# Kernel tuning notes

Hardware: AMD Instinct MI355X
Metric: run time of the kernel (lower is better)

The kernel has to match this reference:

```python
import jax, jax.numpy as jnp
import numpy as np
from jax import lax

EPS = 1e-10

def _ln(x, g, b):
    m = x.mean(-1, keepdims=True)
    v = x.var(-1, keepdims=True)
    return (x - m) / jnp.sqrt(v + 1e-5) * g + b

def _gather(t, idx):
    # t: (B, HW, c), idx: (B, HW, d) -> (B, HW, d, c); out[n,i,k,:] = t[n, idx[n,i,k], :]
    return jax.vmap(lambda tn, In: tn[In])(t, idx)

def setup_inputs() -> dict:
    key = jax.random.key(0)
    ks = jax.random.split(key, 20)
    b, v, c, d, h, w, hid, ksz = 2, 2, 128, 64, 64, 64, 256, 5
    hw = h * w
    Bf = b * v  # v_1 == 1 target view per reference view
    std = 0.02
    return {
        'features_mv': jax.random.normal(ks[0], (b, v, c, h, w), jnp.float32),
        'warp_indices': jax.random.randint(ks[1], (Bf, hw, d), 0, hw, jnp.int32),
        'depth_prob': jax.random.uniform(ks[2], (Bf, hw, d), jnp.float32),
        'ln1_g': jnp.ones((c,), jnp.float32), 'ln1_b': jnp.zeros((c,), jnp.float32),
        'wq': jax.random.normal(ks[3], (c, c), jnp.float32) * std, 'bq': jnp.zeros((c,), jnp.float32),
        'wk': jax.random.normal(ks[4], (c, c), jnp.float32) * std, 'bk': jnp.zeros((c,), jnp.float32),
        'wv': jax.random.normal(ks[5], (c, c), jnp.float32) * std, 'bv': jnp.zeros((c,), jnp.float32),
        'k_pe': jax.random.normal(ks[6], (1, 1, d), jnp.float32) * std,
        'v_pe': jax.random.normal(ks[7], (1, 1, d), jnp.float32) * std,
        'rpe': jax.random.normal(ks[8], (1, 1, d), jnp.float32) * std,
        'proj_w': jax.random.normal(ks[9], (c, c), jnp.float32) * std, 'proj_b': jnp.zeros((c,), jnp.float32),
        'ln2_g': jnp.ones((c,), jnp.float32), 'ln2_b': jnp.zeros((c,), jnp.float32),
        'fc1_w': jax.random.normal(ks[10], (c, hid), jnp.float32) * std, 'fc1_b': jnp.zeros((hid,), jnp.float32),
        'dw_w': jax.random.normal(ks[11], (hid, 1, ksz, ksz), jnp.float32) * std, 'dw_b': jnp.zeros((hid,), jnp.float32),
        'fc2_w': jax.random.normal(ks[12], (hid, c), jnp.float32) * std, 'fc2_b': jnp.zeros((c,), jnp.float32),
    }

def reference(features_mv, warp_indices, depth_prob, ln1_g, ln1_b, wq, bq, wk, bk, wv, bv,
              k_pe, v_pe, rpe, proj_w, proj_b, ln2_g, ln2_b, fc1_w, fc1_b, dw_w, dw_b, fc2_w, fc2_b):
    b, v, c, h, w = features_mv.shape
    hw = h * w
    hid = fc1_w.shape[1]
    scale = c ** (-0.5)  # num_heads = 1 -> head_dim = dim

    # (b v) (h w) c
    x = features_mv.reshape(b * v, c, hw).transpose(0, 2, 1)
    shortcut = x
    xn = _ln(x, ln1_g, ln1_b)
    q = xn @ wq + bq
    k = xn @ wk + bk
    vv = xn @ wv + bv

    # nn pairing: v=2, v_1=1 -> each reference view attends the other view
    Q = (q.reshape(b, v, hw, c) * scale).reshape(b * v, hw, c)
    K = k.reshape(b, v, hw, c)[:, ::-1].reshape(b * v, hw, c)
    V = vv.reshape(b, v, hw, c)[:, ::-1].reshape(b * v, hw, c)

    # SMM_QmK: cost[n,i,k] = sum_c Q[n,i,c] * K[n, idx[n,i,k], c]
    Kg = _gather(K, warp_indices)                       # (B, hw, d, c)
    cost = jnp.einsum('bic,bikc->bik', Q, Kg)
    Q_pe = Q.sum(-1, keepdims=True)                     # (B, hw, 1)
    cost = cost + Q_pe * k_pe + rpe                     # broadcast (1,1,d)

    # (Sim_UNet similarity refinement omitted: UNetModel source unavailable; identity here)
    attn = jax.nn.softmax(cost, axis=-1)
    attn = attn * depth_prob
    attn = (attn + EPS) / (attn.sum(-1, keepdims=True) + EPS)

    # SMM_AmV: out[n,i,c] = sum_k attn[n,i,k] * V[n, idx[n,i,k], c]
    Vg = _gather(V, warp_indices)                       # (B, hw, d, c)
    out = jnp.einsum('bik,bikc->bic', attn, Vg)
    out = out + (attn * v_pe).sum(-1, keepdims=True)

    # projection + residual (v_1 == 1 so B == b*v)
    x = shortcut + (out @ proj_w + proj_b)

    # ConvFFN residual branch
    xn2 = _ln(x, ln2_g, ln2_b)
    y = jax.nn.gelu(xn2 @ fc1_w + fc1_b, approximate=False)
    yi = y.transpose(0, 2, 1).reshape(b * v, hid, h, w)
    yc = lax.conv_general_dilated(yi, dw_w, (1, 1), 'SAME', feature_group_count=hid,
                                  dimension_numbers=('NCHW', 'OIHW', 'NCHW'))
    yc = jax.nn.gelu(yc + dw_b[None, :, None, None], approximate=False)
    y = y + yc.reshape(b * v, hid, hw).transpose(0, 2, 1)
    y = y @ fc2_w + fc2_b
    return x + y
```

## Files before the change

### kernel.cpp

```cpp
#include <hip/hip_runtime.h>
#include <math.h>

#define TOK   16384
#define HW    4096
#define C     128
#define D     64
#define HID   256

constexpr float LN_EPS = 1e-5f;
constexpr float EPS_R  = 1e-10f;
constexpr float QSCALE = 0.08838834764831845f;

typedef __attribute__((ext_vector_type(8))) short  bf16x8;
typedef __attribute__((ext_vector_type(4))) float  f32x4;
typedef __attribute__((ext_vector_type(2))) _Float16 half2v;
#define MFMA16(a, b, c) __builtin_amdgcn_mfma_f32_16x16x32_bf16((a), (b), (c), 0, 0, 0)

__device__ __forceinline__ float bflo(unsigned u) { return __uint_as_float(u << 16); }
__device__ __forceinline__ float bfhi(unsigned u) { return __uint_as_float(u & 0xffff0000u); }
__device__ __forceinline__ float bfu(unsigned short u) { return __uint_as_float((unsigned)u << 16); }
__device__ __forceinline__ unsigned short f2bf(float f) {
  unsigned u = __float_as_uint(f);
  unsigned r = (u + 0x7fffu + ((u >> 16) & 1u)) >> 16;
  return (unsigned short)r;
}
__device__ __forceinline__ unsigned short f2h(float f) {
  _Float16 h = (_Float16)f;
  unsigned short r;
  __builtin_memcpy(&r, &h, 2);
  return r;
}
__device__ __forceinline__ float gelu_exact(float x) {
  return 0.5f * x * (1.0f + erff(x * 0.7071067811865476f));
}

union U4H { uint4 v; half2v h[4]; };
union U1H { unsigned v; half2v h; };

#if __has_builtin(__builtin_amdgcn_fdot2)
__device__ __forceinline__ float dot2h(half2v a, half2v b, float c) {
  return __builtin_amdgcn_fdot2(a, b, c, false);
}
#else
__device__ __forceinline__ float dot2h(half2v a, half2v b, float c) {
  return c + (float)a.x * (float)b.x + (float)a.y * (float)b.y;
}
#endif

__global__ __launch_bounds__(256) void k_prepln1(const float* __restrict__ wq,
    const float* __restrict__ wk, const float* __restrict__ wv,
    const float* __restrict__ pw, const float* __restrict__ f1w,
    const float* __restrict__ f2w, unsigned short* __restrict__ wt,
    const float* __restrict__ feat, const float* __restrict__ g,
    const float* __restrict__ b, unsigned short* __restrict__ xnb) {
  __shared__ float tile[64][C + 1];
  int bidx = blockIdx.x;
  if (bidx < 512) {
    int id = bidx * 256 + threadIdx.x;
    if (id < 16384) {
      int n = id >> 7, k = id & 127;
      wt[id] = f2bf(wq[k * 128 + n]);
    } else if (id < 32768) {
      int e = id - 16384; int n = e >> 7, k = e & 127;
      wt[id] = f2bf(wk[k * 128 + n]);
    } else if (id < 49152) {
      int e = id - 32768; int n = e >> 7, k = e & 127;
      wt[id] = f2bf(wv[k * 128 + n]);
    } else if (id < 65536) {
      int e = id - 49152; int n = e >> 7, k = e & 127;
      wt[id] = f2bf(pw[k * 128 + n]);
    } else if (id < 98304) {
      int e = id - 65536; int n = e >> 7, k = e & 127;
      wt[id] = f2bf(f1w[k * 256 + n]);
    } else {
      int e = id - 98304; int n = e >> 8, k = e & 255;
      wt[id] = f2bf(f2w[k * 128 + n]);
    }
    return;
  }
  int t0 = (bidx - 512) * 64;
  int n = t0 / HW, i0 = t0 % HW;
  int tid = threadIdx.x;
  const float* fb = feat + (size_t)n * C * HW;
  for (int e = tid; e < 64 * C; e += 256) {
    int ch = e >> 6, ii = e & 63;
    tile[ii][ch] = fb[(size_t)ch * HW + i0 + ii];
  }
  __syncthreads();
  int wave = tid >> 6, lane = tid & 63;
  for (int tkn = wave; tkn < 64; tkn += 4) {
    float a0 = tile[tkn][lane];
    float a1 = tile[tkn][lane + 64];
    float s = a0 + a1;
    for (int off = 32; off; off >>= 1) s += __shfl_xor(s, off, 64);
    float mean = s * (1.0f / 128.0f);
    float d0 = a0 - mean, d1 = a1 - mean;
    float v = d0 * d0 + d1 * d1;
    for (int off = 32; off; off >>= 1) v += __shfl_xor(v, off, 64);
    float rstd = rsqrtf(v * (1.0f / 128.0f) + LN_EPS);
    size_t ro = (size_t)(t0 + tkn) * C;
    xnb[ro + lane]      = f2bf(d0 * rstd * g[lane] + b[lane]);
    xnb[ro + lane + 64] = f2bf(d1 * rstd * g[lane + 64] + b[lane + 64]);
  }
}

__global__ __launch_bounds__(256) void k_qkv(const unsigned short* __restrict__ xnb,
    const unsigned short* __restrict__ wt,
    const float* __restrict__ bq, const float* __restrict__ bk,
    const float* __restrict__ bv, unsigned short* __restrict__ qh,
    unsigned short* __restrict__ ksw, unsigned short* __restrict__ vsw) {
  int w = threadIdx.x >> 6, lane = threadIdx.x & 63;
  int q4 = lane >> 4, m = lane & 15;
  int t0 = blockIdx.x * 64 + w * 16;
  int wsel = blockIdx.y;
  const unsigned short* Wt = wt + wsel * 16384;
  const unsigned short* ap = xnb + (size_t)(t0 + m) * C + q4 * 8;
  bf16x8 a[4];
  #pragma unroll
  for (int ks = 0; ks < 4; ks++) a[ks] = *(const bf16x8*)(ap + ks * 32);
  f32x4 acc[8];
  #pragma unroll
  for (int nt = 0; nt < 8; nt++) acc[nt] = (f32x4){0.f, 0.f, 0.f, 0.f};
  #pragma unroll
  for (int nt = 0; nt < 8; nt++) {
    const unsigned short* bp = Wt + (size_t)(nt * 16 + m) * C + q4 * 8;
    #pragma unroll
    for (int ks = 0; ks < 4; ks++) {
      bf16x8 bfrag = *(const bf16x8*)(bp + ks * 32);
      acc[nt] = MFMA16(a[ks], bfrag, acc[nt]);
    }
  }
  const float* B = (wsel == 0) ? bq : ((wsel == 1) ? bk : bv);
  float sc = (wsel == 0) ? QSCALE : 1.0f;
  unsigned short* O = (wsel == 0) ? qh : ((wsel == 1) ? ksw : vsw);
  int n = t0 >> 12, i0 = t0 & 4095;
  int base = (wsel == 0) ? t0 : (((n ^ 1) << 12) + i0);
  #pragma unroll
  for (int nt = 0; nt < 8; nt++) {
    int col = nt * 16 + m;
    float bb = B[col];
    #pragma unroll
    for (int reg = 0; reg < 4; reg++) {
      int row = base + q4 * 4 + reg;
      O[(size_t)row * C + col] = f2h((acc[nt][reg] + bb) * sc);
    }
  }
}

__global__ __launch_bounds__(256) void k_attn_proj_fc1(
    const unsigned short* __restrict__ qh, const unsigned short* __restrict__ ksw,
    const unsigned short* __restrict__ vsw, const int* __restrict__ widx,
    const float* __restrict__ dprob, const float* __restrict__ kpe,
    const float* __restrict__ vpe, const float* __restrict__ rpe,
    const unsigned short* __restrict__ wt, const float* __restrict__ pb,
    const float* __restrict__ feat, float* __restrict__ xio,
    const float* __restrict__ g2, const float* __restrict__ b2,
    const float* __restrict__ f1b, unsigned short* __restrict__ y) {
  __shared__ unsigned short axn[16 * C];
  __shared__ float ps1[4][16];
  __shared__ float ps2[4][16];
  int lane = threadIdx.x & 63;
  int wave = threadIdx.x >> 6;
  int bid = blockIdx.x;
  int n = (bid >> 1) & 3;
  int within = ((bid >> 3) << 1) | (bid & 1);
  int T0 = n * HW + within * 16;
  const unsigned short* Kb = ksw + (size_t)n * HW * C;
  const unsigned short* Vb = vsw + (size_t)n * HW * C;
  int gg = lane >> 3, s = lane & 7;
  half2v ones = {(_Float16)1.0f, (_Float16)1.0f};

  for (int tj = 0; tj < 4; ++tj) {
    int token = T0 + wave * 4 + tj;
    int myidx = widx[(size_t)token * D + lane];
    float mydp = dprob[(size_t)token * D + lane];
    half2v qreg[8];
    {
      const unsigned short* qp = qh + (size_t)token * C + s * 16;
      U4H qa, qb2;
      qa.v = *(const uint4*)(qp);
      qb2.v = *(const uint4*)(qp + 8);
      #pragma unroll
      for (int i = 0; i < 4; i++) { qreg[i] = qa.h[i]; qreg[4 + i] = qb2.h[i]; }
    }
    float qpe = 0.f;
    #pragma unroll
    for (int i = 0; i < 8; i++) qpe = dot2h(qreg[i], ones, qpe);
    qpe += __shfl_xor(qpe, 1, 64);
    qpe += __shfl_xor(qpe, 2, 64);
    qpe += __shfl_xor(qpe, 4, 64);
    int rowv[8];
    #pragma unroll
    for (int pass = 0; pass < 8; ++pass)
      rowv[pass] = __shfl(myidx, pass * 8 + gg, 64);
    uint4 ka[8], kb[8];
    #pragma unroll
    for (int pass = 0; pass < 8; ++pass) {
      const unsigned short* kr = Kb + (size_t)rowv[pass] * C + s * 16;
      ka[pass] = *(const uint4*)(kr);
      kb[pass] = *(const uint4*)(kr + 8);
    }
    float mycost = 0.f;
    #pragma unroll
    for (int pass = 0; pass < 8; ++pass) {
      U4H ua, ub;
      ua.v = ka[pass]; ub.v = kb[pass];
      float p = 0.f;
      #pragma unroll
      for (int i = 0; i < 4; i++) p = dot2h(ua.h[i], qreg[i], p);
      #pragma unroll
      for (int i = 0; i < 4; i++) p = dot2h(ub.h[i], qreg[4 + i], p);
      p += __shfl_xor(p, 1, 64);
      p += __shfl_xor(p, 2, 64);
      p += __shfl_xor(p, 4, 64);
      float t = __shfl(p, (lane & 7) << 3, 64);
      if (pass == gg) mycost = t;
    }
    mycost += qpe * kpe[lane] + rpe[lane];
    float mx = mycost;
    for (int off = 32; off; off >>= 1) mx = fmaxf(mx, __shfl_xor(mx, off, 64));
    float e = __expf(mycost - mx);
    float ssum = e;
    for (int off = 32; off; off >>= 1) ssum += __shfl_xor(ssum, off, 64);
    float attn = (e / ssum) * mydp;
    float sren = attn;
    for (int off = 32; off; off >>= 1) sren += __shfl_xor(sren, off, 64);
    attn = (attn + EPS_R) / (sren + EPS_R);
    float vpt = attn * vpe[lane];
    for (int off = 32; off; off >>= 1) vpt += __shfl_xor(vpt, off, 64);
    float o0 = vpt, o1 = vpt;
    unsigned att_u = __float_as_uint(attn);
    #pragma unroll
    for (int blk = 0; blk < 8; ++blk) {
      unsigned vv[8];
      #pragma unroll
      for (int j = 0; j < 8; j++) {
        int row = __builtin_amdgcn_readlane(myidx, blk * 8 + j);
        vv[j] = *(const unsigned*)(Vb + (size_t)row * C + lane * 2);
      }
      #pragma unroll
      for (int j = 0; j < 8; j++) {
        float a = __uint_as_float(__builtin_amdgcn_readlane(att_u, blk * 8 + j));
        U1H h; h.v = vv[j];
        o0 += a * (float)h.h.x;
        o1 += a * (float)h.h.y;
      }
    }
    unsigned pk = (unsigned)f2bf(o0) | ((unsigned)f2bf(o1) << 16);
    int row = wave * 4 + tj;
    int boff = row * 256 + lane * 4;
    boff ^= (row & 15) << 4;
    *(unsigned*)((char*)axn + boff) = pk;
  }
  __syncthreads();

  int q4 = lane >> 4, m = lane & 15;
  bf16x8 a[4];
  #pragma unroll
  for (int ks = 0; ks < 4; ks++) {
    int boff = m * 256 + ks * 64 + q4 * 16;
    boff ^= m << 4;
    a[ks] = *(const bf16x8*)((char*)axn + boff);
  }
  const unsigned short* Wp = wt + 3 * 16384;
  f32x4 acc[2];
  #pragma unroll
  for (int nt = 0; nt < 2; nt++) acc[nt] = (f32x4){0.f, 0.f, 0.f, 0.f};
  #pragma unroll
  for (int nt = 0; nt < 2; nt++) {
    int colt = wave * 32 + nt * 16;
    const unsigned short* bp = Wp + (size_t)(colt + m) * C + q4 * 8;
    #pragma unroll
    for (int ks = 0; ks < 4; ks++) {
      bf16x8 bfrag = *(const bf16x8*)(bp + ks * 32);
      acc[nt] = MFMA16(a[ks], bfrag, acc[nt]);
    }
  }
  int ibase = (T0 & 4095) + q4 * 4;
  float s1[4] = {0.f, 0.f, 0.f, 0.f}, s2[4] = {0.f, 0.f, 0.f, 0.f};
  #pragma unroll
  for (int nt = 0; nt < 2; nt++) {
    int col = wave * 32 + nt * 16 + m;
    float bb = pb[col];
    const float* fp = feat + ((size_t)n * C + col) * HW + ibase;
    #pragma unroll
    for (int reg = 0; reg < 4; reg++) {
      float v = acc[nt][reg] + bb + fp[reg];
      acc[nt][reg] = v;
      s1[reg] += v;
      s2[reg] += v * v;
    }
  }
  #pragma unroll
  for (int reg = 0; reg < 4; reg++) {
    #pragma unroll
    for (int off = 1; off < 16; off <<= 1) {
      s1[reg] += __shfl_xor(s1[reg], off, 64);
      s2[reg] += __shfl_xor(s2[reg], off, 64);
    }
  }
  if (m == 0) {
    #pragma unroll
    for (int reg = 0; reg < 4; reg++) {
      ps1[wave][q4 * 4 + reg] = s1[reg];
      ps2[wave][q4 * 4 + reg] = s2[reg];
    }
  }
  __syncthreads();
  float mean[4], rstd[4];
  #pragma unroll
  for (int reg = 0; reg < 4; reg++) {
    int row = q4 * 4 + reg;
    float t1 = ps1[0][row] + ps1[1][row] + ps1[2][row] + ps1[3][row];
    float t2 = ps2[0][row] + ps2[1][row] + ps2[2][row] + ps2[3][row];
    mean[reg] = t1 * (1.0f / 128.0f);
    float var = t2 * (1.0f / 128.0f) - mean[reg] * mean[reg];
    rstd[reg] = rsqrtf(var + LN_EPS);
  }
  #pragma unroll
  for (int nt = 0; nt < 2; nt++) {
    int col = wave * 32 + nt * 16 + m;
    float gc = g2[col], bc = b2[col];
    #pragma unroll
    for (int reg = 0; reg < 4; reg++) {
      int row = q4 * 4 + reg;
      float v = acc[nt][reg];
      xio[(size_t)(T0 + row) * C + col] = v;
      unsigned short xv = f2bf((v - mean[reg]) * rstd[reg] * gc + bc);
      int boff = row * 256 + col * 2;
      boff ^= (row & 15) << 4;
      *(unsigned short*)((char*)axn + boff) = xv;
    }
  }
  __syncthreads();

  bf16x8 af[4];
  #pragma unroll
  for (int ks = 0; ks < 4; ks++) {
    int boff = m * 256 + ks * 64 + q4 * 16;
    boff ^= m << 4;
    af[ks] = *(const bf16x8*)((char*)axn + boff);
  }
  const unsigned short* Wf = wt + 65536;
  f32x4 acc2[4];
  #pragma unroll
  for (int nt = 0; nt < 4; nt++) acc2[nt] = (f32x4){0.f, 0.f, 0.f, 0.f};
  #pragma unroll
  for (int nt = 0; nt < 4; nt++) {
    int colt = wave * 64 + nt * 16;
    const unsigned short* bp = Wf + (size_t)(colt + m) * C + q4 * 8;
    #pragma unroll
    for (int ks = 0; ks < 4; ks++) {
      bf16x8 bfrag = *(const bf16x8*)(bp + ks * 32);
      acc2[nt] = MFMA16(af[ks], bfrag, acc2[nt]);
    }
  }
  #pragma unroll
  for (int nt = 0; nt < 4; nt++) {
    int col = wave * 64 + nt * 16 + m;
    float bb = f1b[col];
    #pragma unroll
    for (int reg = 0; reg < 4; reg++) {
      int row = T0 + q4 * 4 + reg;
      y[(size_t)row * HID + col] = f2bf(gelu_exact(acc2[nt][reg] + bb));
    }
  }
}

__global__ __launch_bounds__(256) void k_dwconv(const unsigned short* __restrict__ y,
    const float* __restrict__ w, const float* __restrict__ bias,
    unsigned short* __restrict__ ysum) {
  __shared__ float tile[8][401];
  __shared__ float wl[8][25];
  __shared__ float bl[8];
  int bid = blockIdx.x;
  int tile_id = bid & 15;
  int cb = (bid >> 4) & 31;
  int n = bid >> 9;
  int ty = (tile_id >> 2) * 16, tx = (tile_id & 3) * 16;
  int ch0 = cb * 8;
  int tid = threadIdx.x;
  if (tid < 200) wl[tid / 25][tid % 25] = w[(size_t)(ch0 + tid / 25) * 25 + tid % 25];
  if (tid < 8) bl[tid] = bias[ch0 + tid];
  const unsigned short* yb = y + (size_t)n * HW * HID;
  for (int p = tid; p < 400; p += 256) {
    int py = p / 20, px = p % 20;
    int gy = ty + py - 2, gx = tx + px - 2;
    uint4 v = make_uint4(0u, 0u, 0u, 0u);
    if (gy >= 0 && gy < 64 && gx >= 0 && gx < 64)
      v = *(const uint4*)(yb + (size_t)(gy * 64 + gx) * HID + ch0);
    tile[0][p] = bflo(v.x); tile[1][p] = bfhi(v.x);
    tile[2][p] = bflo(v.y); tile[3][p] = bfhi(v.y);
    tile[4][p] = bflo(v.z); tile[5][p] = bfhi(v.z);
    tile[6][p] = bflo(v.w); tile[7][p] = bfhi(v.w);
  }
  __syncthreads();
  int cc = tid & 7;
  int xx = (tid >> 3) & 15;
  int yg = tid >> 7;
  float wreg[25];
  #pragma unroll
  for (int k = 0; k < 25; k++) wreg[k] = wl[cc][k];
  float bb = bl[cc];
  float win[12][5];
  #pragma unroll
  for (int r = 0; r < 12; r++)
    #pragma unroll
    for (int dx = 0; dx < 5; dx++)
      win[r][dx] = tile[cc][(yg * 8 + r) * 20 + xx + dx];
  #pragma unroll
  for (int j = 0; j < 8; ++j) {
    float acc = 0.f;
    #pragma unroll
    for (int dy = 0; dy < 5; ++dy)
      #pragma unroll
      for (int dx = 0; dx < 5; ++dx)
        acc += wreg[dy * 5 + dx] * win[j + dy][dx];
    float o = win[j + 2][2] + gelu_exact(acc + bb);
    int yy = yg * 8 + j;
    ysum[(size_t)(n * HW + (ty + yy) * 64 + tx + xx) * HID + ch0 + cc] = f2bf(o);
  }
}

__global__ __launch_bounds__(256) void k_fc2(const unsigned short* __restrict__ ysum,
    const unsigned short* __restrict__ wt, const float* __restrict__ f2b,
    const float* __restrict__ xio, float* __restrict__ outp) {
  int w = threadIdx.x >> 6, lane = threadIdx.x & 63;
  int q4 = lane >> 4, m = lane & 15;
  int t0 = blockIdx.x * 64 + w * 16;
  int half = blockIdx.y;
  const unsigned short* Wt = wt + 98304;
  const unsigned short* ap = ysum + (size_t)(t0 + m) * HID + q4 * 8;
  bf16x8 a[8];
  #pragma unroll
  for (int ks = 0; ks < 8; ks++) a[ks] = *(const bf16x8*)(ap + ks * 32);
  f32x4 acc[4];
  #pragma unroll
  for (int nt = 0; nt < 4; nt++) acc[nt] = (f32x4){0.f, 0.f, 0.f, 0.f};
  #pragma unroll
  for (int nt = 0; nt < 4; nt++) {
    const unsigned short* bp = Wt + (size_t)(half * 64 + nt * 16 + m) * HID + q4 * 8;
    #pragma unroll
    for (int ks = 0; ks < 8; ks++) {
      bf16x8 bfrag = *(const bf16x8*)(bp + ks * 32);
      acc[nt] = MFMA16(a[ks], bfrag, acc[nt]);
    }
  }
  #pragma unroll
  for (int nt = 0; nt < 4; nt++) {
    int col = half * 64 + nt * 16 + m;
    float bb = f2b[col];
    #pragma unroll
    for (int reg = 0; reg < 4; reg++) {
      int row = t0 + q4 * 4 + reg;
      outp[(size_t)row * C + col] = acc[nt][reg] + bb + xio[(size_t)row * C + col];
    }
  }
}

extern "C" void kernel_launch(void* const* d_in, const int* in_sizes, int n_in,
                              void* d_out, int out_size, void* d_ws, size_t ws_size,
                              hipStream_t stream) {
  (void)in_sizes; (void)n_in; (void)out_size; (void)ws_size;
  const float* feat  = (const float*)d_in[0];
  const int*   widx  = (const int*)d_in[1];
  const float* dprob = (const float*)d_in[2];
  const float* ln1g  = (const float*)d_in[3];
  const float* ln1b  = (const float*)d_in[4];
  const float* wq    = (const float*)d_in[5];
  const float* bq    = (const float*)d_in[6];
  const float* wk    = (const float*)d_in[7];
  const float* bk    = (const float*)d_in[8];
  const float* wv    = (const float*)d_in[9];
  const float* bv    = (const float*)d_in[10];
  const float* kpe   = (const float*)d_in[11];
  const float* vpe   = (const float*)d_in[12];
  const float* rpe   = (const float*)d_in[13];
  const float* pw    = (const float*)d_in[14];
  const float* pb    = (const float*)d_in[15];
  const float* ln2g  = (const float*)d_in[16];
  const float* ln2b  = (const float*)d_in[17];
  const float* f1w   = (const float*)d_in[18];
  const float* f1b   = (const float*)d_in[19];
  const float* dww   = (const float*)d_in[20];
  const float* dwb   = (const float*)d_in[21];
  const float* f2w   = (const float*)d_in[22];
  const float* f2b   = (const float*)d_in[23];

  float* ws = (float*)d_ws;
  const size_t M2 = (size_t)TOK * C;
  float* xio = ws;
  unsigned short* qhb   = (unsigned short*)(ws + M2);
  unsigned short* xnb   = (unsigned short*)(ws + M2 + M2 / 2);
  unsigned short* ksb   = (unsigned short*)(ws + 2 * M2);
  unsigned short* vsb   = (unsigned short*)(ws + 2 * M2 + M2 / 2);
  unsigned short* yb    = (unsigned short*)(ws + 3 * M2);
  unsigned short* ysumb = (unsigned short*)(ws + 4 * M2);
  unsigned short* wtb   = (unsigned short*)(ws + 5 * M2);

  k_prepln1<<<512 + TOK / 64, 256, 0, stream>>>(wq, wk, wv, pw, f1w, f2w, wtb,
                                                feat, ln1g, ln1b, xnb);
  k_qkv   <<<dim3(TOK / 64, 3), 256, 0, stream>>>(xnb, wtb, bq, bk, bv, qhb, ksb, vsb);
  k_attn_proj_fc1<<<TOK / 16, 256, 0, stream>>>(qhb, ksb, vsb, widx, dprob, kpe, vpe,
                                                rpe, wtb, pb, feat, xio, ln2g, ln2b,
                                                f1b, yb);
  k_dwconv<<<2048, 256, 0, stream>>>(yb, dww, dwb, ysumb);
  k_fc2   <<<dim3(TOK / 64, 2), 256, 0, stream>>>(ysumb, wtb, f2b, xio, (float*)d_out);
}
```

Measured before the change: 209.8 us.

## Split attention from proj/fc1, widen grids, and stage dwconv output via LDS

Splits the fused attention+projection+fc1 kernel into a one-token-per-wave attention kernel, which writes its bf16 output to global memory, and a separate proj/fc1 kernel. This gives the gather-heavy attention stage more independent waves for latency hiding. It also halves the per-block work in the LN1 prep, QKV and fc2 kernels so they launch more blocks, and changes the V gather batching from 8 to 16 loads. The depthwise conv now stages its outputs in shared memory and writes them as 16-byte vector stores instead of scattered 2-byte stores. In exchange, the attention output makes an extra round trip through global memory and there is one more kernel launch.

```diff
diff --git a/kernel.cpp b/kernel.cpp
--- a/kernel.cpp
+++ b/kernel.cpp
@@ -53,7 +53,7 @@
     const float* __restrict__ f2w, unsigned short* __restrict__ wt,
     const float* __restrict__ feat, const float* __restrict__ g,
     const float* __restrict__ b, unsigned short* __restrict__ xnb) {
-  __shared__ float tile[64][C + 1];
+  __shared__ float tile[32][C + 1];
   int bidx = blockIdx.x;
   if (bidx < 512) {
     int id = bidx * 256 + threadIdx.x;
@@ -78,17 +78,17 @@
     }
     return;
   }
-  int t0 = (bidx - 512) * 64;
+  int t0 = (bidx - 512) * 32;
   int n = t0 / HW, i0 = t0 % HW;
   int tid = threadIdx.x;
   const float* fb = feat + (size_t)n * C * HW;
-  for (int e = tid; e < 64 * C; e += 256) {
-    int ch = e >> 6, ii = e & 63;
+  for (int e = tid; e < 32 * C; e += 256) {
+    int ch = e >> 5, ii = e & 31;
     tile[ii][ch] = fb[(size_t)ch * HW + i0 + ii];
   }
   __syncthreads();
   int wave = tid >> 6, lane = tid & 63;
-  for (int tkn = wave; tkn < 64; tkn += 4) {
+  for (int tkn = wave; tkn < 32; tkn += 4) {
     float a0 = tile[tkn][lane];
     float a1 = tile[tkn][lane + 64];
     float s = a0 + a1;
@@ -112,18 +112,19 @@
   int w = threadIdx.x >> 6, lane = threadIdx.x & 63;
   int q4 = lane >> 4, m = lane & 15;
   int t0 = blockIdx.x * 64 + w * 16;
-  int wsel = blockIdx.y;
+  int wsel = blockIdx.y >> 1;
+  int hf = blockIdx.y & 1;
   const unsigned short* Wt = wt + wsel * 16384;
   const unsigned short* ap = xnb + (size_t)(t0 + m) * C + q4 * 8;
   bf16x8 a[4];
   #pragma unroll
   for (int ks = 0; ks < 4; ks++) a[ks] = *(const bf16x8*)(ap + ks * 32);
-  f32x4 acc[8];
-  #pragma unroll
-  for (int nt = 0; nt < 8; nt++) acc[nt] = (f32x4){0.f, 0.f, 0.f, 0.f};
-  #pragma unroll
-  for (int nt = 0; nt < 8; nt++) {
-    const unsigned short* bp = Wt + (size_t)(nt * 16 + m) * C + q4 * 8;
+  f32x4 acc[4];
+  #pragma unroll
+  for (int nt = 0; nt < 4; nt++) acc[nt] = (f32x4){0.f, 0.f, 0.f, 0.f};
+  #pragma unroll
+  for (int nt = 0; nt < 4; nt++) {
+    const unsigned short* bp = Wt + (size_t)(hf * 64 + nt * 16 + m) * C + q4 * 8;
     #pragma unroll
     for (int ks = 0; ks < 4; ks++) {
       bf16x8 bfrag = *(const bf16x8*)(bp + ks * 32);
@@ -136,8 +137,8 @@
   int n = t0 >> 12, i0 = t0 & 4095;
   int base = (wsel == 0) ? t0 : (((n ^ 1) << 12) + i0);
   #pragma unroll
-  for (int nt = 0; nt < 8; nt++) {
-    int col = nt * 16 + m;
+  for (int nt = 0; nt < 4; nt++) {
+    int col = hf * 64 + nt * 16 + m;
     float bb = B[col];
     #pragma unroll
     for (int reg = 0; reg < 4; reg++) {
@@ -147,121 +148,118 @@
   }
 }
 
-__global__ __launch_bounds__(256) void k_attn_proj_fc1(
-    const unsigned short* __restrict__ qh, const unsigned short* __restrict__ ksw,
-    const unsigned short* __restrict__ vsw, const int* __restrict__ widx,
-    const float* __restrict__ dprob, const float* __restrict__ kpe,
-    const float* __restrict__ vpe, const float* __restrict__ rpe,
-    const unsigned short* __restrict__ wt, const float* __restrict__ pb,
-    const float* __restrict__ feat, float* __restrict__ xio,
-    const float* __restrict__ g2, const float* __restrict__ b2,
-    const float* __restrict__ f1b, unsigned short* __restrict__ y) {
+__global__ __launch_bounds__(256) void k_attn(const unsigned short* __restrict__ qh,
+    const unsigned short* __restrict__ ksw, const unsigned short* __restrict__ vsw,
+    const int* __restrict__ widx, const float* __restrict__ dprob,
+    const float* __restrict__ kpe, const float* __restrict__ vpe,
+    const float* __restrict__ rpe, unsigned short* __restrict__ aoutb) {
+  int lane = threadIdx.x & 63;
+  int wave = threadIdx.x >> 6;
+  int bid = blockIdx.x;
+  int n = (bid >> 1) & 3;
+  int within = ((bid >> 3) << 1) | (bid & 1);
+  int token = n * HW + within * 4 + wave;
+  const unsigned short* Kb = ksw + (size_t)n * HW * C;
+  const unsigned short* Vb = vsw + (size_t)n * HW * C;
+  int g = lane >> 3, s = lane & 7;
+  int myidx = widx[(size_t)token * D + lane];
+  float mydp = dprob[(size_t)token * D + lane];
+  half2v qreg[8];
+  {
+    const unsigned short* qp = qh + (size_t)token * C + s * 16;
+    U4H qa, qb2;
+    qa.v = *(const uint4*)(qp);
+    qb2.v = *(const uint4*)(qp + 8);
+    #pragma unroll
+    for (int i = 0; i < 4; i++) { qreg[i] = qa.h[i]; qreg[4 + i] = qb2.h[i]; }
+  }
+  half2v ones = {(_Float16)1.0f, (_Float16)1.0f};
+  float qpe = 0.f;
+  #pragma unroll
+  for (int i = 0; i < 8; i++) qpe = dot2h(qreg[i], ones, qpe);
+  qpe += __shfl_xor(qpe, 1, 64);
+  qpe += __shfl_xor(qpe, 2, 64);
+  qpe += __shfl_xor(qpe, 4, 64);
+  int rowv[8];
+  #pragma unroll
+  for (int pass = 0; pass < 8; ++pass)
+    rowv[pass] = __shfl(myidx, pass * 8 + g, 64);
+  uint4 ka[8], kb[8];
+  #pragma unroll
+  for (int pass = 0; pass < 8; ++pass) {
+    const unsigned short* kr = Kb + (size_t)rowv[pass] * C + s * 16;
+    ka[pass] = *(const uint4*)(kr);
+    kb[pass] = *(const uint4*)(kr + 8);
+  }
+  float mycost = 0.f;
+  #pragma unroll
+  for (int pass = 0; pass < 8; ++pass) {
+    U4H ua, ub;
+    ua.v = ka[pass]; ub.v = kb[pass];
+    float p = 0.f;
+    #pragma unroll
+    for (int i = 0; i < 4; i++) p = dot2h(ua.h[i], qreg[i], p);
+    #pragma unroll
+    for (int i = 0; i < 4; i++) p = dot2h(ub.h[i], qreg[4 + i], p);
+    p += __shfl_xor(p, 1, 64);
+    p += __shfl_xor(p, 2, 64);
+    p += __shfl_xor(p, 4, 64);
+    float t = __shfl(p, (lane & 7) << 3, 64);
+    if (pass == g) mycost = t;
+  }
+  mycost += qpe * kpe[lane] + rpe[lane];
+  float mx = mycost;
+  for (int off = 32; off; off >>= 1) mx = fmaxf(mx, __shfl_xor(mx, off, 64));
+  float e = __expf(mycost - mx);
+  float ssum = e;
+  for (int off = 32; off; off >>= 1) ssum += __shfl_xor(ssum, off, 64);
+  float attn = (e / ssum) * mydp;
+  float s2 = attn;
+  for (int off = 32; off; off >>= 1) s2 += __shfl_xor(s2, off, 64);
+  attn = (attn + EPS_R) / (s2 + EPS_R);
+  float vpt = attn * vpe[lane];
+  for (int off = 32; off; off >>= 1) vpt += __shfl_xor(vpt, off, 64);
+  float o0 = vpt, o1 = vpt;
+  unsigned att_u = __float_as_uint(attn);
+  #pragma unroll
+  for (int blk = 0; blk < 4; ++blk) {
+    unsigned vv[16];
+    #pragma unroll
+    for (int j = 0; j < 16; j++) {
+      int row = __builtin_amdgcn_readlane(myidx, blk * 16 + j);
+      vv[j] = *(const unsigned*)(Vb + (size_t)row * C + lane * 2);
+    }
+    #pragma unroll
+    for (int j = 0; j < 16; j++) {
+      float a = __uint_as_float(__builtin_amdgcn_readlane(att_u, blk * 16 + j));
+      U1H h; h.v = vv[j];
+      o0 += a * (float)h.h.x;
+      o1 += a * (float)h.h.y;
+    }
+  }
+  unsigned pk = (unsigned)f2bf(o0) | ((unsigned)f2bf(o1) << 16);
+  *(unsigned*)(aoutb + (size_t)token * C + lane * 2) = pk;
+}
+
+__global__ __launch_bounds__(256) void k_projfc1(
+    const unsigned short* __restrict__ aoutb, const unsigned short* __restrict__ wt,
+    const float* __restrict__ pb, const float* __restrict__ feat,
+    float* __restrict__ xio, const float* __restrict__ g2,
+    const float* __restrict__ b2, const float* __restrict__ f1b,
+    unsigned short* __restrict__ y) {
   __shared__ unsigned short axn[16 * C];
   __shared__ float ps1[4][16];
   __shared__ float ps2[4][16];
   int lane = threadIdx.x & 63;
   int wave = threadIdx.x >> 6;
-  int bid = blockIdx.x;
-  int n = (bid >> 1) & 3;
-  int within = ((bid >> 3) << 1) | (bid & 1);
-  int T0 = n * HW + within * 16;
-  const unsigned short* Kb = ksw + (size_t)n * HW * C;
-  const unsigned short* Vb = vsw + (size_t)n * HW * C;
-  int gg = lane >> 3, s = lane & 7;
-  half2v ones = {(_Float16)1.0f, (_Float16)1.0f};
-
-  for (int tj = 0; tj < 4; ++tj) {
-    int token = T0 + wave * 4 + tj;
-    int myidx = widx[(size_t)token * D + lane];
-    float mydp = dprob[(size_t)token * D + lane];
-    half2v qreg[8];
-    {
-      const unsigned short* qp = qh + (size_t)token * C + s * 16;
-      U4H qa, qb2;
-      qa.v = *(const uint4*)(qp);
-      qb2.v = *(const uint4*)(qp + 8);
-      #pragma unroll
-      for (int i = 0; i < 4; i++) { qreg[i] = qa.h[i]; qreg[4 + i] = qb2.h[i]; }
-    }
-    float qpe = 0.f;
-    #pragma unroll
-    for (int i = 0; i < 8; i++) qpe = dot2h(qreg[i], ones, qpe);
-    qpe += __shfl_xor(qpe, 1, 64);
-    qpe += __shfl_xor(qpe, 2, 64);
-    qpe += __shfl_xor(qpe, 4, 64);
-    int rowv[8];
-    #pragma unroll
-    for (int pass = 0; pass < 8; ++pass)
-      rowv[pass] = __shfl(myidx, pass * 8 + gg, 64);
-    uint4 ka[8], kb[8];
-    #pragma unroll
-    for (int pass = 0; pass < 8; ++pass) {
-      const unsigned short* kr = Kb + (size_t)rowv[pass] * C + s * 16;
-      ka[pass] = *(const uint4*)(kr);
-      kb[pass] = *(const uint4*)(kr + 8);
-    }
-    float mycost = 0.f;
-    #pragma unroll
-    for (int pass = 0; pass < 8; ++pass) {
-      U4H ua, ub;
-      ua.v = ka[pass]; ub.v = kb[pass];
-      float p = 0.f;
-      #pragma unroll
-      for (int i = 0; i < 4; i++) p = dot2h(ua.h[i], qreg[i], p);
-      #pragma unroll
-      for (int i = 0; i < 4; i++) p = dot2h(ub.h[i], qreg[4 + i], p);
-      p += __shfl_xor(p, 1, 64);
-      p += __shfl_xor(p, 2, 64);
-      p += __shfl_xor(p, 4, 64);
-      float t = __shfl(p, (lane & 7) << 3, 64);
-      if (pass == gg) mycost = t;
-    }
-    mycost += qpe * kpe[lane] + rpe[lane];
-    float mx = mycost;
-    for (int off = 32; off; off >>= 1) mx = fmaxf(mx, __shfl_xor(mx, off, 64));
-    float e = __expf(mycost - mx);
-    float ssum = e;
-    for (int off = 32; off; off >>= 1) ssum += __shfl_xor(ssum, off, 64);
-    float attn = (e / ssum) * mydp;
-    float sren = attn;
-    for (int off = 32; off; off >>= 1) sren += __shfl_xor(sren, off, 64);
-    attn = (attn + EPS_R) / (sren + EPS_R);
-    float vpt = attn * vpe[lane];
-    for (int off = 32; off; off >>= 1) vpt += __shfl_xor(vpt, off, 64);
-    float o0 = vpt, o1 = vpt;
-    unsigned att_u = __float_as_uint(attn);
-    #pragma unroll
-    for (int blk = 0; blk < 8; ++blk) {
-      unsigned vv[8];
-      #pragma unroll
-      for (int j = 0; j < 8; j++) {
-        int row = __builtin_amdgcn_readlane(myidx, blk * 8 + j);
-        vv[j] = *(const unsigned*)(Vb + (size_t)row * C + lane * 2);
-      }
-      #pragma unroll
-      for (int j = 0; j < 8; j++) {
-        float a = __uint_as_float(__builtin_amdgcn_readlane(att_u, blk * 8 + j));
-        U1H h; h.v = vv[j];
-        o0 += a * (float)h.h.x;
-        o1 += a * (float)h.h.y;
-      }
-    }
-    unsigned pk = (unsigned)f2bf(o0) | ((unsigned)f2bf(o1) << 16);
-    int row = wave * 4 + tj;
-    int boff = row * 256 + lane * 4;
-    boff ^= (row & 15) << 4;
-    *(unsigned*)((char*)axn + boff) = pk;
-  }
-  __syncthreads();
-
+  int T0 = blockIdx.x * 16;
+  int n = T0 >> 12;
   int q4 = lane >> 4, m = lane & 15;
+
+  const unsigned short* ap = aoutb + (size_t)(T0 + m) * C + q4 * 8;
   bf16x8 a[4];
   #pragma unroll
-  for (int ks = 0; ks < 4; ks++) {
-    int boff = m * 256 + ks * 64 + q4 * 16;
-    boff ^= m << 4;
-    a[ks] = *(const bf16x8*)((char*)axn + boff);
-  }
+  for (int ks = 0; ks < 4; ks++) a[ks] = *(const bf16x8*)(ap + ks * 32);
   const unsigned short* Wp = wt + 3 * 16384;
   f32x4 acc[2];
   #pragma unroll
@@ -373,6 +371,7 @@
   __shared__ float tile[8][401];
   __shared__ float wl[8][25];
   __shared__ float bl[8];
+  __shared__ unsigned short outl[256][8];
   int bid = blockIdx.x;
   int tile_id = bid & 15;
   int cb = (bid >> 4) & 31;
@@ -418,7 +417,14 @@
         acc += wreg[dy * 5 + dx] * win[j + dy][dx];
     float o = win[j + 2][2] + gelu_exact(acc + bb);
     int yy = yg * 8 + j;
-    ysum[(size_t)(n * HW + (ty + yy) * 64 + tx + xx) * HID + ch0 + cc] = f2bf(o);
+    outl[yy * 16 + xx][cc] = f2bf(o);
+  }
+  __syncthreads();
+  {
+    int p = tid;
+    int yy = p >> 4, xx2 = p & 15;
+    uint4 val = *(const uint4*)outl[p];
+    *(uint4*)(ysum + (size_t)(n * HW + (ty + yy) * 64 + tx + xx2) * HID + ch0) = val;
   }
 }
 
@@ -428,18 +434,18 @@
   int w = threadIdx.x >> 6, lane = threadIdx.x & 63;
   int q4 = lane >> 4, m = lane & 15;
   int t0 = blockIdx.x * 64 + w * 16;
-  int half = blockIdx.y;
+  int quarter = blockIdx.y;
   const unsigned short* Wt = wt + 98304;
   const unsigned short* ap = ysum + (size_t)(t0 + m) * HID + q4 * 8;
   bf16x8 a[8];
   #pragma unroll
   for (int ks = 0; ks < 8; ks++) a[ks] = *(const bf16x8*)(ap + ks * 32);
-  f32x4 acc[4];
-  #pragma unroll
-  for (int nt = 0; nt < 4; nt++) acc[nt] = (f32x4){0.f, 0.f, 0.f, 0.f};
-  #pragma unroll
-  for (int nt = 0; nt < 4; nt++) {
-    const unsigned short* bp = Wt + (size_t)(half * 64 + nt * 16 + m) * HID + q4 * 8;
+  f32x4 acc[2];
+  #pragma unroll
+  for (int nt = 0; nt < 2; nt++) acc[nt] = (f32x4){0.f, 0.f, 0.f, 0.f};
+  #pragma unroll
+  for (int nt = 0; nt < 2; nt++) {
+    const unsigned short* bp = Wt + (size_t)(quarter * 32 + nt * 16 + m) * HID + q4 * 8;
     #pragma unroll
     for (int ks = 0; ks < 8; ks++) {
       bf16x8 bfrag = *(const bf16x8*)(bp + ks * 32);
@@ -447,8 +453,8 @@
     }
   }
   #pragma unroll
-  for (int nt = 0; nt < 4; nt++) {
-    int col = half * 64 + nt * 16 + m;
+  for (int nt = 0; nt < 2; nt++) {
+    int col = quarter * 32 + nt * 16 + m;
     float bb = f2b[col];
     #pragma unroll
     for (int reg = 0; reg < 4; reg++) {
@@ -494,16 +500,16 @@
   unsigned short* xnb   = (unsigned short*)(ws + M2 + M2 / 2);
   unsigned short* ksb   = (unsigned short*)(ws + 2 * M2);
   unsigned short* vsb   = (unsigned short*)(ws + 2 * M2 + M2 / 2);
-  unsigned short* yb    = (unsigned short*)(ws + 3 * M2);
-  unsigned short* ysumb = (unsigned short*)(ws + 4 * M2);
-  unsigned short* wtb   = (unsigned short*)(ws + 5 * M2);
-
-  k_prepln1<<<512 + TOK / 64, 256, 0, stream>>>(wq, wk, wv, pw, f1w, f2w, wtb,
-                                                feat, ln1g, ln1b, xnb);
-  k_qkv   <<<dim3(TOK / 64, 3), 256, 0, stream>>>(xnb, wtb, bq, bk, bv, qhb, ksb, vsb);
-  k_attn_proj_fc1<<<TOK / 16, 256, 0, stream>>>(qhb, ksb, vsb, widx, dprob, kpe, vpe,
-                                                rpe, wtb, pb, feat, xio, ln2g, ln2b,
-                                                f1b, yb);
-  k_dwconv<<<2048, 256, 0, stream>>>(yb, dww, dwb, ysumb);
-  k_fc2   <<<dim3(TOK / 64, 2), 256, 0, stream>>>(ysumb, wtb, f2b, xio, (float*)d_out);
-}
+  unsigned short* aoutb = (unsigned short*)(ws + 3 * M2);
+  unsigned short* yb    = (unsigned short*)(ws + 3 * M2 + M2 / 2);
+  unsigned short* ysumb = (unsigned short*)(ws + 4 * M2 + M2 / 2);
+  unsigned short* wtb   = (unsigned short*)(ws + 5 * M2 + M2 / 2);
+
+  k_prepln1<<<1024, 256, 0, stream>>>(wq, wk, wv, pw, f1w, f2w, wtb,
+                                      feat, ln1g, ln1b, xnb);
+  k_qkv    <<<dim3(TOK / 64, 6), 256, 0, stream>>>(xnb, wtb, bq, bk, bv, qhb, ksb, vsb);
+  k_attn   <<<TOK / 4, 256, 0, stream>>>(qhb, ksb, vsb, widx, dprob, kpe, vpe, rpe, aoutb);
+  k_projfc1<<<TOK / 16, 256, 0, stream>>>(aoutb, wtb, pb, feat, xio, ln2g, ln2b, f1b, yb);
+  k_dwconv <<<2048, 256, 0, stream>>>(yb, dww, dwb, ysumb);
+  k_fc2    <<<dim3(TOK / 64, 4), 256, 0, stream>>>(ysumb, wtb, f2b, xio, (float*)d_out);
+}
```

After: 205.4 us. 2.1% less time.

## Split GEMM grids finer, prefetch V rows early, stage dwconv output in LDS

Applied to the files above, without the earlier changes.

Several independent changes. The LN1 prep and the qkv and fc2 GEMMs are split into more, smaller blocks so more waves run at once. The attention kernel issues the first half of the V gathers before computing the cost and gets a launch bound of 3 blocks, trading extra register pressure for earlier latency hiding. The depthwise conv stages its bf16 outputs in shared memory so each pixel is written as one 16-byte store instead of scattered 2-byte stores.

```diff
diff --git a/kernel.cpp b/kernel.cpp
--- a/kernel.cpp
+++ b/kernel.cpp
@@ -18,7 +18,6 @@
 
 __device__ __forceinline__ float bflo(unsigned u) { return __uint_as_float(u << 16); }
 __device__ __forceinline__ float bfhi(unsigned u) { return __uint_as_float(u & 0xffff0000u); }
-__device__ __forceinline__ float bfu(unsigned short u) { return __uint_as_float((unsigned)u << 16); }
 __device__ __forceinline__ unsigned short f2bf(float f) {
   unsigned u = __float_as_uint(f);
   unsigned r = (u + 0x7fffu + ((u >> 16) & 1u)) >> 16;
@@ -53,7 +52,7 @@
     const float* __restrict__ f2w, unsigned short* __restrict__ wt,
     const float* __restrict__ feat, const float* __restrict__ g,
     const float* __restrict__ b, unsigned short* __restrict__ xnb) {
-  __shared__ float tile[64][C + 1];
+  __shared__ float tile[32][C + 1];
   int bidx = blockIdx.x;
   if (bidx < 512) {
     int id = bidx * 256 + threadIdx.x;
@@ -78,17 +77,17 @@
     }
     return;
   }
-  int t0 = (bidx - 512) * 64;
+  int t0 = (bidx - 512) * 32;
   int n = t0 / HW, i0 = t0 % HW;
   int tid = threadIdx.x;
   const float* fb = feat + (size_t)n * C * HW;
-  for (int e = tid; e < 64 * C; e += 256) {
-    int ch = e >> 6, ii = e & 63;
+  for (int e = tid; e < 32 * C; e += 256) {
+    int ch = e >> 5, ii = e & 31;
     tile[ii][ch] = fb[(size_t)ch * HW + i0 + ii];
   }
   __syncthreads();
   int wave = tid >> 6, lane = tid & 63;
-  for (int tkn = wave; tkn < 64; tkn += 4) {
+  for (int tkn = wave; tkn < 32; tkn += 4) {
     float a0 = tile[tkn][lane];
     float a1 = tile[tkn][lane + 64];
     float s = a0 + a1;
@@ -112,18 +111,19 @@
   int w = threadIdx.x >> 6, lane = threadIdx.x & 63;
   int q4 = lane >> 4, m = lane & 15;
   int t0 = blockIdx.x * 64 + w * 16;
-  int wsel = blockIdx.y;
+  int wsel = blockIdx.y >> 1;
+  int hf = blockIdx.y & 1;
   const unsigned short* Wt = wt + wsel * 16384;
   const unsigned short* ap = xnb + (size_t)(t0 + m) * C + q4 * 8;
   bf16x8 a[4];
   #pragma unroll
   for (int ks = 0; ks < 4; ks++) a[ks] = *(const bf16x8*)(ap + ks * 32);
-  f32x4 acc[8];
-  #pragma unroll
-  for (int nt = 0; nt < 8; nt++) acc[nt] = (f32x4){0.f, 0.f, 0.f, 0.f};
-  #pragma unroll
-  for (int nt = 0; nt < 8; nt++) {
-    const unsigned short* bp = Wt + (size_t)(nt * 16 + m) * C + q4 * 8;
+  f32x4 acc[4];
+  #pragma unroll
+  for (int nt = 0; nt < 4; nt++) acc[nt] = (f32x4){0.f, 0.f, 0.f, 0.f};
+  #pragma unroll
+  for (int nt = 0; nt < 4; nt++) {
+    const unsigned short* bp = Wt + (size_t)(hf * 64 + nt * 16 + m) * C + q4 * 8;
     #pragma unroll
     for (int ks = 0; ks < 4; ks++) {
       bf16x8 bfrag = *(const bf16x8*)(bp + ks * 32);
@@ -136,8 +136,8 @@
   int n = t0 >> 12, i0 = t0 & 4095;
   int base = (wsel == 0) ? t0 : (((n ^ 1) << 12) + i0);
   #pragma unroll
-  for (int nt = 0; nt < 8; nt++) {
-    int col = nt * 16 + m;
+  for (int nt = 0; nt < 4; nt++) {
+    int col = hf * 64 + nt * 16 + m;
     float bb = B[col];
     #pragma unroll
     for (int reg = 0; reg < 4; reg++) {
@@ -147,7 +147,7 @@
   }
 }
 
-__global__ __launch_bounds__(256) void k_attn_proj_fc1(
+__global__ __launch_bounds__(256, 3) void k_attn_proj_fc1(
     const unsigned short* __restrict__ qh, const unsigned short* __restrict__ ksw,
     const unsigned short* __restrict__ vsw, const int* __restrict__ widx,
     const float* __restrict__ dprob, const float* __restrict__ kpe,
@@ -183,23 +183,29 @@
       #pragma unroll
       for (int i = 0; i < 4; i++) { qreg[i] = qa.h[i]; qreg[4 + i] = qb2.h[i]; }
     }
+    int rowv[8];
+    #pragma unroll
+    for (int pass = 0; pass < 8; ++pass)
+      rowv[pass] = __shfl(myidx, pass * 8 + gg, 64);
+    uint4 ka[8], kb[8];
+    #pragma unroll
+    for (int pass = 0; pass < 8; ++pass) {
+      const unsigned short* kr = Kb + (size_t)rowv[pass] * C + s * 16;
+      ka[pass] = *(const uint4*)(kr);
+      kb[pass] = *(const uint4*)(kr + 8);
+    }
+    unsigned vv0[32];
+    #pragma unroll
+    for (int j = 0; j < 32; j++) {
+      int row = __builtin_amdgcn_readlane(myidx, j);
+      vv0[j] = *(const unsigned*)(Vb + (size_t)row * C + lane * 2);
+    }
     float qpe = 0.f;
     #pragma unroll
     for (int i = 0; i < 8; i++) qpe = dot2h(qreg[i], ones, qpe);
     qpe += __shfl_xor(qpe, 1, 64);
     qpe += __shfl_xor(qpe, 2, 64);
     qpe += __shfl_xor(qpe, 4, 64);
-    int rowv[8];
-    #pragma unroll
-    for (int pass = 0; pass < 8; ++pass)
-      rowv[pass] = __shfl(myidx, pass * 8 + gg, 64);
-    uint4 ka[8], kb[8];
-    #pragma unroll
-    for (int pass = 0; pass < 8; ++pass) {
-      const unsigned short* kr = Kb + (size_t)rowv[pass] * C + s * 16;
-      ka[pass] = *(const uint4*)(kr);
-      kb[pass] = *(const uint4*)(kr + 8);
-    }
     float mycost = 0.f;
     #pragma unroll
     for (int pass = 0; pass < 8; ++pass) {
@@ -223,28 +229,32 @@
     float ssum = e;
     for (int off = 32; off; off >>= 1) ssum += __shfl_xor(ssum, off, 64);
     float attn = (e / ssum) * mydp;
-    float sren = attn;
-    for (int off = 32; off; off >>= 1) sren += __shfl_xor(sren, off, 64);
-    attn = (attn + EPS_R) / (sren + EPS_R);
+    float s2 = attn;
+    for (int off = 32; off; off >>= 1) s2 += __shfl_xor(s2, off, 64);
+    attn = (attn + EPS_R) / (s2 + EPS_R);
     float vpt = attn * vpe[lane];
     for (int off = 32; off; off >>= 1) vpt += __shfl_xor(vpt, off, 64);
     float o0 = vpt, o1 = vpt;
     unsigned att_u = __float_as_uint(attn);
-    #pragma unroll
-    for (int blk = 0; blk < 8; ++blk) {
-      unsigned vv[8];
-      #pragma unroll
-      for (int j = 0; j < 8; j++) {
-        int row = __builtin_amdgcn_readlane(myidx, blk * 8 + j);
-        vv[j] = *(const unsigned*)(Vb + (size_t)row * C + lane * 2);
-      }
-      #pragma unroll
-      for (int j = 0; j < 8; j++) {
-        float a = __uint_as_float(__builtin_amdgcn_readlane(att_u, blk * 8 + j));
-        U1H h; h.v = vv[j];
-        o0 += a * (float)h.h.x;
-        o1 += a * (float)h.h.y;
-      }
+    unsigned vv1[32];
+    #pragma unroll
+    for (int j = 0; j < 32; j++) {
+      int row = __builtin_amdgcn_readlane(myidx, 32 + j);
+      vv1[j] = *(const unsigned*)(Vb + (size_t)row * C + lane * 2);
+    }
+    #pragma unroll
+    for (int j = 0; j < 32; j++) {
+      float a = __uint_as_float(__builtin_amdgcn_readlane(att_u, j));
+      U1H h; h.v = vv0[j];
+      o0 += a * (float)h.h.x;
+      o1 += a * (float)h.h.y;
+    }
+    #pragma unroll
+    for (int j = 0; j < 32; j++) {
+      float a = __uint_as_float(__builtin_amdgcn_readlane(att_u, 32 + j));
+      U1H h; h.v = vv1[j];
+      o0 += a * (float)h.h.x;
+      o1 += a * (float)h.h.y;
     }
     unsigned pk = (unsigned)f2bf(o0) | ((unsigned)f2bf(o1) << 16);
     int row = wave * 4 + tj;
@@ -277,7 +287,7 @@
     }
   }
   int ibase = (T0 & 4095) + q4 * 4;
-  float s1[4] = {0.f, 0.f, 0.f, 0.f}, s2[4] = {0.f, 0.f, 0.f, 0.f};
+  float s1[4] = {0.f, 0.f, 0.f, 0.f}, s2b[4] = {0.f, 0.f, 0.f, 0.f};
   #pragma unroll
   for (int nt = 0; nt < 2; nt++) {
     int col = wave * 32 + nt * 16 + m;
@@ -288,7 +298,7 @@
       float v = acc[nt][reg] + bb + fp[reg];
       acc[nt][reg] = v;
       s1[reg] += v;
-      s2[reg] += v * v;
+      s2b[reg] += v * v;
     }
   }
   #pragma unroll
@@ -296,14 +306,14 @@
     #pragma unroll
     for (int off = 1; off < 16; off <<= 1) {
       s1[reg] += __shfl_xor(s1[reg], off, 64);
-      s2[reg] += __shfl_xor(s2[reg], off, 64);
+      s2b[reg] += __shfl_xor(s2b[reg], off, 64);
     }
   }
   if (m == 0) {
     #pragma unroll
     for (int reg = 0; reg < 4; reg++) {
       ps1[wave][q4 * 4 + reg] = s1[reg];
-      ps2[wave][q4 * 4 + reg] = s2[reg];
+      ps2[wave][q4 * 4 + reg] = s2b[reg];
     }
   }
   __syncthreads();
@@ -373,6 +383,7 @@
   __shared__ float tile[8][401];
   __shared__ float wl[8][25];
   __shared__ float bl[8];
+  __shared__ unsigned short outl[256][8];
   int bid = blockIdx.x;
   int tile_id = bid & 15;
   int cb = (bid >> 4) & 31;
@@ -418,7 +429,14 @@
         acc += wreg[dy * 5 + dx] * win[j + dy][dx];
     float o = win[j + 2][2] + gelu_exact(acc + bb);
     int yy = yg * 8 + j;
-    ysum[(size_t)(n * HW + (ty + yy) * 64 + tx + xx) * HID + ch0 + cc] = f2bf(o);
+    outl[yy * 16 + xx][cc] = f2bf(o);
+  }
+  __syncthreads();
+  {
+    int p = tid;
+    int yy = p >> 4, xx2 = p & 15;
+    uint4 val = *(const uint4*)outl[p];
+    *(uint4*)(ysum + (size_t)(n * HW + (ty + yy) * 64 + tx + xx2) * HID + ch0) = val;
   }
 }
 
@@ -428,18 +446,18 @@
   int w = threadIdx.x >> 6, lane = threadIdx.x & 63;
   int q4 = lane >> 4, m = lane & 15;
   int t0 = blockIdx.x * 64 + w * 16;
-  int half = blockIdx.y;
+  int quarter = blockIdx.y;
   const unsigned short* Wt = wt + 98304;
   const unsigned short* ap = ysum + (size_t)(t0 + m) * HID + q4 * 8;
   bf16x8 a[8];
   #pragma unroll
   for (int ks = 0; ks < 8; ks++) a[ks] = *(const bf16x8*)(ap + ks * 32);
-  f32x4 acc[4];
-  #pragma unroll
-  for (int nt = 0; nt < 4; nt++) acc[nt] = (f32x4){0.f, 0.f, 0.f, 0.f};
-  #pragma unroll
-  for (int nt = 0; nt < 4; nt++) {
-    const unsigned short* bp = Wt + (size_t)(half * 64 + nt * 16 + m) * HID + q4 * 8;
+  f32x4 acc[2];
+  #pragma unroll
+  for (int nt = 0; nt < 2; nt++) acc[nt] = (f32x4){0.f, 0.f, 0.f, 0.f};
+  #pragma unroll
+  for (int nt = 0; nt < 2; nt++) {
+    const unsigned short* bp = Wt + (size_t)(quarter * 32 + nt * 16 + m) * HID + q4 * 8;
     #pragma unroll
     for (int ks = 0; ks < 8; ks++) {
       bf16x8 bfrag = *(const bf16x8*)(bp + ks * 32);
@@ -447,8 +465,8 @@
     }
   }
   #pragma unroll
-  for (int nt = 0; nt < 4; nt++) {
-    int col = half * 64 + nt * 16 + m;
+  for (int nt = 0; nt < 2; nt++) {
+    int col = quarter * 32 + nt * 16 + m;
     float bb = f2b[col];
     #pragma unroll
     for (int reg = 0; reg < 4; reg++) {
@@ -498,12 +516,12 @@
   unsigned short* ysumb = (unsigned short*)(ws + 4 * M2);
   unsigned short* wtb   = (unsigned short*)(ws + 5 * M2);
 
-  k_prepln1<<<512 + TOK / 64, 256, 0, stream>>>(wq, wk, wv, pw, f1w, f2w, wtb,
-                                                feat, ln1g, ln1b, xnb);
-  k_qkv   <<<dim3(TOK / 64, 3), 256, 0, stream>>>(xnb, wtb, bq, bk, bv, qhb, ksb, vsb);
+  k_prepln1<<<1024, 256, 0, stream>>>(wq, wk, wv, pw, f1w, f2w, wtb,
+                                      feat, ln1g, ln1b, xnb);
+  k_qkv    <<<dim3(TOK / 64, 6), 256, 0, stream>>>(xnb, wtb, bq, bk, bv, qhb, ksb, vsb);
   k_attn_proj_fc1<<<TOK / 16, 256, 0, stream>>>(qhb, ksb, vsb, widx, dprob, kpe, vpe,
                                                 rpe, wtb, pb, feat, xio, ln2g, ln2b,
                                                 f1b, yb);
-  k_dwconv<<<2048, 256, 0, stream>>>(yb, dww, dwb, ysumb);
-  k_fc2   <<<dim3(TOK / 64, 2), 256, 0, stream>>>(ysumb, wtb, f2b, xio, (float*)d_out);
-}
+  k_dwconv <<<2048, 256, 0, stream>>>(yb, dww, dwb, ysumb);
+  k_fc2    <<<dim3(TOK / 64, 4), 256, 0, stream>>>(ysumb, wtb, f2b, xio, (float*)d_out);
+}
```

After: 201.2 us. 4.1% less time.
